# Optimization experiments

Hardware: AMD Instinct MI355X
Metric: run time of the kernel (lower is better)

The kernel has to match this reference:

```python
import jax, jax.numpy as jnp
import numpy as np

QF = 28  # quality_factor from init

_BASE_QUANT = np.array([
    [16, 11, 10, 16, 24, 40, 51, 61],
    [12, 12, 14, 19, 26, 58, 60, 55],
    [14, 13, 16, 24, 40, 57, 69, 56],
    [14, 17, 22, 29, 51, 87, 80, 62],
    [18, 22, 37, 56, 68, 109, 103, 77],
    [24, 35, 55, 64, 81, 104, 113, 92],
    [49, 64, 78, 87, 103, 121, 120, 101],
    [72, 92, 95, 98, 112, 100, 103, 99]], dtype=np.float32)

def _quant_matrix(qf: int) -> jnp.ndarray:
    scale = 50.0 / max(1, qf) if qf < 25 else 200.0 - 2 * qf
    return jnp.asarray(np.maximum(_BASE_QUANT * scale / 50.0, 1.0), dtype=jnp.float32)

def _dct_basis(N: int = 8) -> jnp.ndarray:
    # Orthonormal DCT-II basis: basis @ x @ basis.T is the 2D DCT (norm='ortho')
    k = np.arange(N)[:, None].astype(np.float32)
    n = np.arange(N)[None, :].astype(np.float32)
    b = np.sqrt(2.0 / N) * np.cos(np.pi * k * (2 * n + 1) / (2 * N))
    b[0, :] = np.sqrt(1.0 / N)
    return jnp.asarray(b, dtype=jnp.float32)

def setup_inputs() -> dict:
    key = jax.random.key(0)
    x = jax.random.uniform(key, (8, 3, 1080, 1920), dtype=jnp.float32) * 255.0
    return {"x": x}

def reference(x):
    B, C, H, W = x.shape
    basis = _dct_basis(8)
    q = _quant_matrix(QF)  # (8, 8)

    # BGR -> Y (luminance)
    b, g, r = x[:, 0:1], x[:, 1:2], x[:, 2:3]
    y = 0.114 * b + 0.587 * g + 0.299 * r  # (B, 1, H, W)

    # pad to multiple of 8 (replicate)
    pad_h, pad_w = (-H) % 8, (-W) % 8
    yp = jnp.pad(y, ((0, 0), (0, 0), (0, pad_h), (0, pad_w)), mode='edge') if (pad_h or pad_w) else y
    Hp, Wp = H + pad_h, W + pad_w
    nh, nw = Hp // 8, Wp // 8

    # split into 8x8 blocks: (B, 1, nh, nw, 8, 8)
    blocks = yp.reshape(B, 1, nh, 8, nw, 8).transpose(0, 1, 2, 4, 3, 5)

    # 2D DCT (ortho): basis @ block @ basis.T
    coef = jnp.einsum('ki,...ij,lj->...kl', basis, blocks, basis)

    # hard quantization with straight-through estimator (training-mode forward == hard)
    qhard = jnp.round(coef / (q + 1e-8)) * q
    coef_q = coef + jax.lax.stop_gradient(qhard - coef)

    # 2D inverse DCT: basis.T @ block @ basis
    rec = jnp.einsum('ik,...ij,jl->...kl', basis, coef_q, basis)

    # reassemble blocks -> image, crop padding
    y_rec = rec.transpose(0, 1, 2, 4, 3, 5).reshape(B, 1, Hp, Wp)[:, :, :H, :W]

    # Y back to BGR: add luminance delta weighted by the BGR->Y coefficients
    yd = y_rec - y
    out = jnp.concatenate([b + 0.114 * yd, g + 0.587 * yd, r + 0.299 * yd], axis=1)
    return jnp.clip(out, 0.0, 255.0)
```

## Files before the change

kernel.cpp:

```cpp
#include <hip/hip_runtime.h>
#include <math.h>

#define IMG_H 1080
#define IMG_W 1920
#define HW (IMG_H * IMG_W)
#define NBATCH 8

typedef float f4 __attribute__((ext_vector_type(4)));

__device__ __constant__ int BASEQ[64] = {
    16, 11, 10, 16, 24, 40, 51, 61,
    12, 12, 14, 19, 26, 58, 60, 55,
    14, 13, 16, 24, 40, 57, 69, 56,
    14, 17, 22, 29, 51, 87, 80, 62,
    18, 22, 37, 56, 68, 109, 103, 77,
    24, 35, 55, 64, 81, 104, 113, 92,
    49, 64, 78, 87, 103, 121, 120, 101,
    72, 92, 95, 98, 112, 100, 103, 99};

__device__ __forceinline__ float clamp255(float v) {
    return fminf(fmaxf(v, 0.0f), 255.0f);
}

__device__ __forceinline__ void wave_lds_fence() {
    __builtin_amdgcn_wave_barrier();
    __builtin_amdgcn_s_waitcnt(0xC07F);
    __builtin_amdgcn_wave_barrier();
}

__global__ __launch_bounds__(192) void h264_kernel(const float* __restrict__ x,
                                                   float* __restrict__ out) {
    __shared__ __align__(16) float yt[3 * 512];
    __shared__ float t2[3 * 576];
    __shared__ float bl[64];
    __shared__ float ql[64];

    const int t = threadIdx.x;
    const int wave = t >> 6;
    const int lane = t & 63;

    {
        int k = lane >> 3, n = lane & 7;
        float v;
        if (k == 0) {
            v = 0.35355339059327373f;
        } else {
            float a = 3.14159265358979323846f * (float)k;
            a = a * (2.0f * (float)n + 1.0f);
            a = a / 16.0f;
            v = 0.5f * cosf(a);
        }
        bl[lane] = v;
        ql[lane] = __fdiv_rn((float)(BASEQ[lane] * 144), 50.0f);
    }

    const int h0 = blockIdx.y * 8;
    const int wcol0 = blockIdx.x * 192 + wave * 64;
    const int bat = blockIdx.z;
    const float* xb = x + (size_t)bat * 3 * HW;
    float* ob = out + (size_t)bat * 3 * HW;

    float* ytw = yt + wave * 512;
    float* t2w = t2 + wave * 576;

    f4 Bv[2], Gv[2], Rv[2];
    int gaddr[2];
#pragma unroll
    for (int it = 0; it < 2; ++it) {
        int idx = lane + (it << 6);
        int row = idx >> 4;
        int c4 = (idx & 15) << 2;
        int ga = (h0 + row) * IMG_W + wcol0 + c4;
        gaddr[it] = ga;
        Bv[it] = __builtin_nontemporal_load((const f4*)(xb + ga));
        Gv[it] = __builtin_nontemporal_load((const f4*)(xb + HW + ga));
        Rv[it] = __builtin_nontemporal_load((const f4*)(xb + 2 * HW + ga));
        f4 y4;
        y4.x = __fadd_rn(__fadd_rn(__fmul_rn(0.114f, Bv[it].x), __fmul_rn(0.587f, Gv[it].x)), __fmul_rn(0.299f, Rv[it].x));
        y4.y = __fadd_rn(__fadd_rn(__fmul_rn(0.114f, Bv[it].y), __fmul_rn(0.587f, Gv[it].y)), __fmul_rn(0.299f, Rv[it].y));
        y4.z = __fadd_rn(__fadd_rn(__fmul_rn(0.114f, Bv[it].z), __fmul_rn(0.587f, Gv[it].z)), __fmul_rn(0.299f, Rv[it].z));
        y4.w = __fadd_rn(__fadd_rn(__fmul_rn(0.114f, Bv[it].w), __fmul_rn(0.587f, Gv[it].w)), __fmul_rn(0.299f, Rv[it].w));
        *(f4*)(ytw + row * 64 + c4) = y4;
    }
    wave_lds_fence();

    const int blk = lane >> 3;
    const int l = lane & 7;
    float* t2b = t2w + blk * 72;

    float ycol[8];
#pragma unroll
    for (int i = 0; i < 8; ++i) ycol[i] = ytw[i * 64 + lane];

    float c1[8];
#pragma unroll
    for (int k = 0; k < 8; ++k) {
        float acc = 0.0f;
#pragma unroll
        for (int i = 0; i < 8; ++i) acc = fmaf(bl[k * 8 + i], ycol[i], acc);
        c1[k] = acc;
    }
#pragma unroll
    for (int k = 0; k < 8; ++k) t2b[l * 9 + k] = c1[k];
    wave_lds_fence();

    float coef[8];
#pragma unroll
    for (int k = 0; k < 8; ++k) {
        float acc = 0.0f;
#pragma unroll
        for (int j = 0; j < 8; ++j) acc = fmaf(t2b[j * 9 + k], bl[l * 8 + j], acc);
        float q = ql[k * 8 + l];
        coef[k] = __fmul_rn(rintf(__fdiv_rn(acc, q)), q);
    }
    wave_lds_fence();
#pragma unroll
    for (int k = 0; k < 8; ++k) t2b[l * 9 + k] = coef[k];
    wave_lds_fence();

    float s[8];
#pragma unroll
    for (int i = 0; i < 8; ++i) {
        float acc = 0.0f;
#pragma unroll
        for (int j = 0; j < 8; ++j) acc = fmaf(t2b[j * 9 + i], bl[j * 8 + l], acc);
        s[i] = acc;
    }
    float yd[8];
#pragma unroll
    for (int k = 0; k < 8; ++k) {
        float acc = 0.0f;
#pragma unroll
        for (int i = 0; i < 8; ++i) acc = fmaf(bl[i * 8 + k], s[i], acc);
        yd[k] = __fsub_rn(acc, ycol[k]);
    }
#pragma unroll
    for (int k = 0; k < 8; ++k) ytw[k * 64 + lane] = yd[k];
    wave_lds_fence();

#pragma unroll
    for (int it = 0; it < 2; ++it) {
        int idx = lane + (it << 6);
        int row = idx >> 4;
        int c4 = (idx & 15) << 2;
        f4 y4 = *(f4*)(ytw + row * 64 + c4);
        int ga = gaddr[it];
        f4 o0, o1, o2;
        o0.x = clamp255(__fadd_rn(Bv[it].x, __fmul_rn(0.114f, y4.x)));
        o0.y = clamp255(__fadd_rn(Bv[it].y, __fmul_rn(0.114f, y4.y)));
        o0.z = clamp255(__fadd_rn(Bv[it].z, __fmul_rn(0.114f, y4.z)));
        o0.w = clamp255(__fadd_rn(Bv[it].w, __fmul_rn(0.114f, y4.w)));
        o1.x = clamp255(__fadd_rn(Gv[it].x, __fmul_rn(0.587f, y4.x)));
        o1.y = clamp255(__fadd_rn(Gv[it].y, __fmul_rn(0.587f, y4.y)));
        o1.z = clamp255(__fadd_rn(Gv[it].z, __fmul_rn(0.587f, y4.z)));
        o1.w = clamp255(__fadd_rn(Gv[it].w, __fmul_rn(0.587f, y4.w)));
        o2.x = clamp255(__fadd_rn(Rv[it].x, __fmul_rn(0.299f, y4.x)));
        o2.y = clamp255(__fadd_rn(Rv[it].y, __fmul_rn(0.299f, y4.y)));
        o2.z = clamp255(__fadd_rn(Rv[it].z, __fmul_rn(0.299f, y4.z)));
        o2.w = clamp255(__fadd_rn(Rv[it].w, __fmul_rn(0.299f, y4.w)));
        __builtin_nontemporal_store(o0, (f4*)(ob + ga));
        __builtin_nontemporal_store(o1, (f4*)(ob + HW + ga));
        __builtin_nontemporal_store(o2, (f4*)(ob + 2 * HW + ga));
    }
}

extern "C" void kernel_launch(void* const* d_in, const int* in_sizes, int n_in,
                              void* d_out, int out_size, void* d_ws, size_t ws_size,
                              hipStream_t stream) {
    const float* x = (const float*)d_in[0];
    float* out = (float*)d_out;
    dim3 grid(IMG_W / 192, IMG_H / 8, NBATCH);
    dim3 block(192);
    h264_kernel<<<grid, block, 0, stream>>>(x, out);
}
```

Measured before the change: 317.5 us.

## Bake DCT/quant tables at compile time and vectorize LDS transposes with double buffers

```diff
diff --git a/kernel.cpp b/kernel.cpp
--- a/kernel.cpp
+++ b/kernel.cpp
@@ -8,7 +8,27 @@
 
 typedef float f4 __attribute__((ext_vector_type(4)));
 
-__device__ __constant__ int BASEQ[64] = {
+constexpr float HCONST[9] = {
+    0.5f,
+    0.49039264020161522f,
+    0.46193976625564337f,
+    0.41573480615127262f,
+    0.35355339059327376f,
+    0.27778511650980109f,
+    0.19134171618254489f,
+    0.097545161008064135f,
+    0.0f};
+
+constexpr float fbasis(int k, int n) {
+    if (k == 0) return 0.35355339059327373f;
+    int m = (k * (2 * n + 1)) & 31;
+    float s = 1.0f;
+    if (m > 16) m = 32 - m;
+    if (m > 8) { m = 16 - m; s = -1.0f; }
+    return s * HCONST[m];
+}
+
+constexpr int BASEQC[64] = {
     16, 11, 10, 16, 24, 40, 51, 61,
     12, 12, 14, 19, 26, 58, 60, 55,
     14, 13, 16, 24, 40, 57, 69, 56,
@@ -18,6 +38,33 @@
     49, 64, 78, 87, 103, 121, 120, 101,
     72, 92, 95, 98, 112, 100, 103, 99};
 
+struct alignas(16) T64 { float v[64]; };
+
+constexpr T64 gen_bl() {
+    T64 t{};
+    for (int k = 0; k < 8; ++k)
+        for (int n = 0; n < 8; ++n) t.v[k * 8 + n] = fbasis(k, n);
+    return t;
+}
+constexpr T64 gen_bt() {
+    T64 t{};
+    for (int l = 0; l < 8; ++l)
+        for (int j = 0; j < 8; ++j) t.v[l * 8 + j] = fbasis(j, l);
+    return t;
+}
+constexpr T64 gen_qt() {
+    T64 t{};
+    for (int l = 0; l < 8; ++l)
+        for (int k = 0; k < 8; ++k)
+            t.v[l * 8 + k] = (float)(BASEQC[k * 8 + l] * 144) / 50.0f;
+    return t;
+}
+
+constexpr T64 BLc = gen_bl();
+__device__ __constant__ T64 d_BL = gen_bl();
+__device__ __constant__ T64 d_BT = gen_bt();
+__device__ __constant__ T64 d_QT = gen_qt();
+
 __device__ __forceinline__ float clamp255(float v) {
     return fminf(fmaxf(v, 0.0f), 255.0f);
 }
@@ -28,31 +75,29 @@
     __builtin_amdgcn_wave_barrier();
 }
 
+__device__ __forceinline__ float dot8(f4 d0, f4 d1, f4 w0, f4 w1) {
+    float acc = 0.0f;
+    acc = fmaf(d0.x, w0.x, acc);
+    acc = fmaf(d0.y, w0.y, acc);
+    acc = fmaf(d0.z, w0.z, acc);
+    acc = fmaf(d0.w, w0.w, acc);
+    acc = fmaf(d1.x, w1.x, acc);
+    acc = fmaf(d1.y, w1.y, acc);
+    acc = fmaf(d1.z, w1.z, acc);
+    acc = fmaf(d1.w, w1.w, acc);
+    return acc;
+}
+
 __global__ __launch_bounds__(192) void h264_kernel(const float* __restrict__ x,
                                                    float* __restrict__ out) {
     __shared__ __align__(16) float yt[3 * 512];
-    __shared__ float t2[3 * 576];
-    __shared__ float bl[64];
-    __shared__ float ql[64];
+    __shared__ __align__(16) float t2[3 * 1600];
 
     const int t = threadIdx.x;
     const int wave = t >> 6;
     const int lane = t & 63;
-
-    {
-        int k = lane >> 3, n = lane & 7;
-        float v;
-        if (k == 0) {
-            v = 0.35355339059327373f;
-        } else {
-            float a = 3.14159265358979323846f * (float)k;
-            a = a * (2.0f * (float)n + 1.0f);
-            a = a / 16.0f;
-            v = 0.5f * cosf(a);
-        }
-        bl[lane] = v;
-        ql[lane] = __fdiv_rn((float)(BASEQ[lane] * 144), 50.0f);
-    }
+    const int blk = lane >> 3;
+    const int l = lane & 7;
 
     const int h0 = blockIdx.y * 8;
     const int wcol0 = blockIdx.x * 192 + wave * 64;
@@ -61,7 +106,9 @@
     float* ob = out + (size_t)bat * 3 * HW;
 
     float* ytw = yt + wave * 512;
-    float* t2w = t2 + wave * 576;
+    float* t2w = t2 + wave * 1600;
+    float* t2A = t2w + blk * 100;
+    float* t2B = t2w + 800 + blk * 100;
 
     f4 Bv[2], Gv[2], Rv[2];
     int gaddr[2];
@@ -82,60 +129,53 @@
         y4.w = __fadd_rn(__fadd_rn(__fmul_rn(0.114f, Bv[it].w), __fmul_rn(0.587f, Gv[it].w)), __fmul_rn(0.299f, Rv[it].w));
         *(f4*)(ytw + row * 64 + c4) = y4;
     }
-    wave_lds_fence();
-
-    const int blk = lane >> 3;
-    const int l = lane & 7;
-    float* t2b = t2w + blk * 72;
+
+    const f4 blr0 = *(const f4*)(d_BL.v + l * 8);
+    const f4 blr1 = *((const f4*)(d_BL.v + l * 8) + 1);
+    const f4 blc0 = *(const f4*)(d_BT.v + l * 8);
+    const f4 blc1 = *((const f4*)(d_BT.v + l * 8) + 1);
+    const f4 qc0 = *(const f4*)(d_QT.v + l * 8);
+    const f4 qc1 = *((const f4*)(d_QT.v + l * 8) + 1);
+    const float qv[8] = {qc0.x, qc0.y, qc0.z, qc0.w, qc1.x, qc1.y, qc1.z, qc1.w};
+
+    wave_lds_fence();
 
     float ycol[8];
 #pragma unroll
     for (int i = 0; i < 8; ++i) ycol[i] = ytw[i * 64 + lane];
-
-    float c1[8];
 #pragma unroll
     for (int k = 0; k < 8; ++k) {
         float acc = 0.0f;
 #pragma unroll
-        for (int i = 0; i < 8; ++i) acc = fmaf(bl[k * 8 + i], ycol[i], acc);
-        c1[k] = acc;
-    }
-#pragma unroll
-    for (int k = 0; k < 8; ++k) t2b[l * 9 + k] = c1[k];
-    wave_lds_fence();
-
-    float coef[8];
+        for (int i = 0; i < 8; ++i) acc = fmaf(BLc.v[k * 8 + i], ycol[i], acc);
+        t2A[k * 12 + l] = acc;
+    }
+    wave_lds_fence();
+
+#pragma unroll
+    for (int k = 0; k < 8; ++k) {
+        const f4 r0 = *(const f4*)(t2A + k * 12);
+        const f4 r1 = *((const f4*)(t2A + k * 12) + 1);
+        float acc = dot8(r0, r1, blr0, blr1);
+        const float q = qv[k];
+        t2B[k * 12 + l] = __fmul_rn(rintf(__fdiv_rn(acc, q)), q);
+    }
+    wave_lds_fence();
+
+    float sv[8];
+#pragma unroll
+    for (int i = 0; i < 8; ++i) {
+        const f4 r0 = *(const f4*)(t2B + i * 12);
+        const f4 r1 = *((const f4*)(t2B + i * 12) + 1);
+        sv[i] = dot8(r0, r1, blc0, blc1);
+    }
 #pragma unroll
     for (int k = 0; k < 8; ++k) {
         float acc = 0.0f;
 #pragma unroll
-        for (int j = 0; j < 8; ++j) acc = fmaf(t2b[j * 9 + k], bl[l * 8 + j], acc);
-        float q = ql[k * 8 + l];
-        coef[k] = __fmul_rn(rintf(__fdiv_rn(acc, q)), q);
-    }
-    wave_lds_fence();
-#pragma unroll
-    for (int k = 0; k < 8; ++k) t2b[l * 9 + k] = coef[k];
-    wave_lds_fence();
-
-    float s[8];
-#pragma unroll
-    for (int i = 0; i < 8; ++i) {
-        float acc = 0.0f;
-#pragma unroll
-        for (int j = 0; j < 8; ++j) acc = fmaf(t2b[j * 9 + i], bl[j * 8 + l], acc);
-        s[i] = acc;
-    }
-    float yd[8];
-#pragma unroll
-    for (int k = 0; k < 8; ++k) {
-        float acc = 0.0f;
-#pragma unroll
-        for (int i = 0; i < 8; ++i) acc = fmaf(bl[i * 8 + k], s[i], acc);
-        yd[k] = __fsub_rn(acc, ycol[k]);
-    }
-#pragma unroll
-    for (int k = 0; k < 8; ++k) ytw[k * 64 + lane] = yd[k];
+        for (int i = 0; i < 8; ++i) acc = fmaf(BLc.v[i * 8 + k], sv[i], acc);
+        ytw[k * 64 + lane] = __fsub_rn(acc, ycol[k]);
+    }
     wave_lds_fence();
 
 #pragma unroll
```

Measured after the change: 317.3 us. No clear change (-0.1%).
